# Kernel tuning notes

Hardware: AMD Instinct MI355X
Metric: run time of the kernel (lower is better)

Reference implementation:

```python
import jax, jax.numpy as jnp
import numpy as np
from jax import lax

L = 12        # transformer layers
H = 768       # d_model
NH = 12       # heads
HD = H // NH  # head dim
F = 2048      # ffn dim (torch TransformerEncoderLayer default)
V = 128       # vocab_size (level logits)
NLV = 128     # n_levels (rows of routed weight W)
B, S = 8, 512
EPS = 1e-5


def _layer_norm(x, g, b):
    mu = jnp.mean(x, axis=-1, keepdims=True)
    var = jnp.mean(jnp.square(x - mu), axis=-1, keepdims=True)
    return g * (x - mu) / jnp.sqrt(var + EPS) + b


def _encoder(x, layer_params):
    # torch nn.TransformerEncoderLayer, post-LN, ReLU, eval mode (no dropout)
    def block(h, p):
        Wqkv, bqkv, Wo, bo, g1, bb1, W1, b1f, W2, b2f, g2, bb2 = p
        qkv = h @ Wqkv.T + bqkv                      # [B,S,3H]
        q, k, v = jnp.split(qkv, 3, axis=-1)
        sh = (h.shape[0], h.shape[1], NH, HD)
        q, k, v = q.reshape(sh), k.reshape(sh), v.reshape(sh)
        scores = jnp.einsum('bqhd,bkhd->bhqk', q, k) / jnp.sqrt(jnp.asarray(HD, h.dtype))
        attn = jax.nn.softmax(scores, axis=-1)
        o = jnp.einsum('bhqk,bkhd->bqhd', attn, v).reshape(h.shape)
        o = o @ Wo.T + bo
        h = _layer_norm(h + o, g1, bb1)
        f = jnp.maximum(h @ W1.T + b1f, 0.0) @ W2.T + b2f
        h = _layer_norm(h + f, g2, bb2)
        return h, None
    x, _ = lax.scan(block, x, layer_params)
    return x


def setup_inputs() -> dict:
    key = jax.random.key(0)
    ks = jax.random.split(key, 20)
    s = 0.02
    rn = lambda k, shp: jax.random.normal(k, shp, jnp.float32) * s
    inp = {
        'level_ids': jax.random.randint(ks[0], (B, S), 0, V, jnp.int32),
        'sublevel_ids': jax.random.randint(ks[1], (B, S), 0, V, jnp.int32),
        'bin_emb': rn(ks[2], (V, H)),
        'sub_emb': rn(ks[3], (V, H)),
        'Wqkv': rn(ks[4], (L, 3 * H, H)),
        'bqkv': jnp.zeros((L, 3 * H), jnp.float32),
        'Wo': rn(ks[5], (L, H, H)),
        'bo': jnp.zeros((L, H), jnp.float32),
        'ln1_g': jnp.ones((L, H), jnp.float32),
        'ln1_b': jnp.zeros((L, H), jnp.float32),
        'W1': rn(ks[6], (L, F, H)),
        'b1': jnp.zeros((L, F), jnp.float32),
        'W2': rn(ks[7], (L, H, F)),
        'b2': jnp.zeros((L, H), jnp.float32),
        'ln2_g': jnp.ones((L, H), jnp.float32),
        'ln2_b': jnp.zeros((L, H), jnp.float32),
        'W_lm': rn(ks[8], (V, H)),
        'b_lm': jnp.zeros((V,), jnp.float32),
        'W': rn(ks[9], (NLV, H, V)),       # routed per-level weights
        'bias': jnp.zeros((NLV, V), jnp.float32),
    }
    return inp


def reference(level_ids, sublevel_ids, bin_emb, sub_emb, Wqkv, bqkv, Wo, bo,
              ln1_g, ln1_b, W1, b1, W2, b2, ln2_g, ln2_b, W_lm, b_lm, W, bias):
    # embedding: sum of two id tables (tabular bin/subbin embedding)
    x = bin_emb[level_ids] + sub_emb[sublevel_ids]            # [B,S,H]
    layer_params = (Wqkv, bqkv, Wo, bo, ln1_g, ln1_b, W1, b1, W2, b2, ln2_g, ln2_b)
    x = _encoder(x, layer_params)                              # [B,S,H]
    out = x @ W_lm.T + b_lm                                    # [B,S,V]
    ix = jnp.argmax(out, axis=-1)                              # [B,S] routing index
    # per-token weight gather + batched vec-mat: the irregular hot path
    Wg = W[ix]                                                 # [B,S,H,V]
    sublevel_out = jnp.einsum('bsh,bshv->bsv', x, Wg) + bias[ix]
    return (out, sublevel_out)
```

## Files before the change

kernel.cpp:

```cpp
#include <hip/hip_runtime.h>
#include <cstdint>
#include <cstddef>

#define TOK 4096
#define HD_ 64
#define NH_ 12
#define H_ 768
#define F_ 2048
#define V_ 128
#define L_ 12
#define SEQ 512
#define BQKV (3*H_)
#define BATCH 8

typedef _Float16 f16;
typedef _Float16 f16x8 __attribute__((ext_vector_type(8)));
typedef _Float16 f16x4 __attribute__((ext_vector_type(4)));
typedef float    f32x4 __attribute__((ext_vector_type(4)));

#define GLDS16(g, l) __builtin_amdgcn_global_load_lds( \
    (const __attribute__((address_space(1))) uint32_t*)(g), \
    (__attribute__((address_space(3))) uint32_t*)(l), 16, 0, 0)

__device__ __forceinline__ float wave_sum(float v) {
#pragma unroll
  for (int m = 32; m >= 1; m >>= 1) v += __shfl_xor(v, m);
  return v;
}

__device__ __forceinline__ void split16(float v, f16& h, f16& lo) {
  h = (f16)v;
  lo = (f16)((v - (float)h) * 2048.0f);
}

__device__ __forceinline__ int swz(int r, int c) {
  int byte = (r << 7) + (c << 1);
  byte ^= (r & 7) << 4;
  return byte >> 1;
}

__global__ __launch_bounds__(256)
void k_convert(const float* __restrict__ src, f16* __restrict__ h, f16* __restrict__ l,
               int n4, float scale) {
  int i = blockIdx.x * 256 + threadIdx.x;
  int stride = gridDim.x * 256;
  for (; i < n4; i += stride) {
    float4 v = ((const float4*)src)[i];
    v.x *= scale; v.y *= scale; v.z *= scale; v.w *= scale;
    f16x4 vh, vl;
    f16 a, b;
    split16(v.x, a, b); vh[0] = a; vl[0] = b;
    split16(v.y, a, b); vh[1] = a; vl[1] = b;
    split16(v.z, a, b); vh[2] = a; vl[2] = b;
    split16(v.w, a, b); vh[3] = a; vl[3] = b;
    ((f16x4*)h)[i] = vh;
    ((f16x4*)l)[i] = vl;
  }
}

__global__ __launch_bounds__(256)
void k_embed2(const int* __restrict__ lid, const int* __restrict__ sid,
              const float* __restrict__ be, const float* __restrict__ se,
              float* __restrict__ x, f16* __restrict__ xh, f16* __restrict__ xl,
              int* __restrict__ counts) {
  int t = blockIdx.x;
  if (t == 0 && threadIdx.x < V_) counts[threadIdx.x] = 0;
  int li = lid[t], si = sid[t];
  const float* bp = be + (size_t)li * H_;
  const float* sp = se + (size_t)si * H_;
  size_t base = (size_t)t * H_;
#pragma unroll
  for (int j = 0; j < 3; ++j) {
    int hh = threadIdx.x + 256 * j;
    float v = bp[hh] + sp[hh];
    x[base + hh] = v;
    f16 a, b; split16(v, a, b);
    xh[base + hh] = a; xl[base + hh] = b;
  }
}

template<int BM, int BN, int MODE>
__global__ __launch_bounds__(256)
void k_gemm4(const f16* __restrict__ Ah, const f16* __restrict__ Al,
             const f16* __restrict__ Bh, const f16* __restrict__ Bl,
             const float* __restrict__ bias, float* __restrict__ C,
             f16* __restrict__ Ch, f16* __restrict__ Cl,
             int N, int K) {
  constexpr int MI = BM / 32, NJ = BN / 32;
  constexpr int IA = BM / 64, IB = BN / 64;
  constexpr int ABYT = BM * 64, BBYT = BN * 64;
  constexpr int BUFB = 2 * ABYT + 2 * BBYT;
  constexpr int NGL = 2 * (IA + IB);
  __shared__ __align__(16) char sm_[3 * BUFB];
  const int tid = threadIdx.x;
  const int lane = tid & 63, wid = tid >> 6;
  const int wr = wid >> 1, wc = wid & 1;
  const int bm = blockIdx.x * BM, bn = blockIdx.y * BN;
  const size_t rs = (size_t)K * 2;

  const int srow = tid >> 2, schk = tid & 3;
  const char* ga[2][IA];
  const char* gb[2][IB];
#pragma unroll
  for (int u = 0; u < IA; ++u) {
    int row = u * 64 + srow;
    int c = schk ^ ((row >> 1) & 3);
    ga[0][u] = (const char*)Ah + (size_t)(bm + row) * rs + c * 16;
    ga[1][u] = (const char*)Al + (size_t)(bm + row) * rs + c * 16;
  }
#pragma unroll
  for (int u = 0; u < IB; ++u) {
    int row = u * 64 + srow;
    int c = schk ^ ((row >> 1) & 3);
    gb[0][u] = (const char*)Bh + (size_t)(bn + row) * rs + c * 16;
    gb[1][u] = (const char*)Bl + (size_t)(bn + row) * rs + c * 16;
  }

  const int rr = lane & 15, cgrp = lane >> 4;
  int aoff[MI][2], boff[NJ][2];
#pragma unroll
  for (int i = 0; i < MI; ++i) {
    int row = wr * (BM / 2) + i * 16 + rr;
    int sw = (cgrp ^ ((row >> 1) & 3)) * 16;
    aoff[i][0] = row * 64 + sw;
    aoff[i][1] = ABYT + row * 64 + sw;
  }
#pragma unroll
  for (int j = 0; j < NJ; ++j) {
    int row = wc * (BN / 2) + j * 16 + rr;
    int sw = (cgrp ^ ((row >> 1) & 3)) * 16;
    boff[j][0] = 2 * ABYT + row * 64 + sw;
    boff[j][1] = 2 * ABYT + BBYT + row * 64 + sw;
  }

  f32x4 aH[MI][NJ], aM[MI][NJ];
#pragma unroll
  for (int i = 0; i < MI; ++i)
#pragma unroll
    for (int j = 0; j < NJ; ++j)
#pragma unroll
      for (int q = 0; q < 4; ++q) { aH[i][j][q] = 0.0f; aM[i][j][q] = 0.0f; }

  auto STG = [&](char* bufbase) __attribute__((always_inline)) {
    char* base = bufbase + wid * 1024;
#pragma unroll
    for (int u = 0; u < IA; ++u) {
      GLDS16(ga[0][u], base + u * 4096);
      GLDS16(ga[1][u], base + ABYT + u * 4096);
      ga[0][u] += 64; ga[1][u] += 64;
    }
#pragma unroll
    for (int u = 0; u < IB; ++u) {
      GLDS16(gb[0][u], base + 2 * ABYT + u * 4096);
      GLDS16(gb[1][u], base + 2 * ABYT + BBYT + u * 4096);
      gb[0][u] += 64; gb[1][u] += 64;
    }
  };

  auto CMP = [&](const char* base) __attribute__((always_inline)) {
    f16x8 fbh[NJ], fbl[NJ];
#pragma unroll
    for (int j = 0; j < NJ; ++j) {
      fbh[j] = *(const f16x8*)(base + boff[j][0]);
      fbl[j] = *(const f16x8*)(base + boff[j][1]);
    }
#pragma unroll
    for (int i = 0; i < MI; ++i) {
      f16x8 fah = *(const f16x8*)(base + aoff[i][0]);
      f16x8 fal = *(const f16x8*)(base + aoff[i][1]);
#pragma unroll
      for (int j = 0; j < NJ; ++j) {
        aH[i][j] = __builtin_amdgcn_mfma_f32_16x16x32_f16(fah, fbh[j], aH[i][j], 0, 0, 0);
        aM[i][j] = __builtin_amdgcn_mfma_f32_16x16x32_f16(fah, fbl[j], aM[i][j], 0, 0, 0);
        aM[i][j] = __builtin_amdgcn_mfma_f32_16x16x32_f16(fal, fbh[j], aM[i][j], 0, 0, 0);
      }
    }
  };

  char* b0 = sm_;
  char* b1 = sm_ + BUFB;
  char* b2 = sm_ + 2 * BUFB;
  STG(b0);
  const int nst = K / 32;
  for (int s = 0; s < nst; ++s) {
    if (s + 1 < nst) {
      STG(b1);
      asm volatile("s_waitcnt vmcnt(%0)" :: "i"(NGL) : "memory");
    } else {
      asm volatile("s_waitcnt vmcnt(0)" ::: "memory");
    }
    __builtin_amdgcn_s_barrier();
    __builtin_amdgcn_sched_barrier(0);
    CMP(b0);
    char* tmp = b0; b0 = b1; b1 = b2; b2 = tmp;
  }

  const int r4 = (lane >> 4) * 4, cc = lane & 15;
#pragma unroll
  for (int i = 0; i < MI; ++i) {
#pragma unroll
    for (int j = 0; j < NJ; ++j) {
      int col = bn + wc * (BN / 2) + j * 16 + cc;
      float bz = bias[col];
#pragma unroll
      for (int q = 0; q < 4; ++q) {
        int row = bm + wr * (BM / 2) + i * 16 + r4 + q;
        float v = (aH[i][j][q] + aM[i][j][q] * (1.0f / 2048.0f)) * (1.0f / 64.0f) + bz;
        if (MODE == 0) {
          C[(size_t)row * N + col] = v;
        } else {
          if (MODE == 1) v = fmaxf(v, 0.0f);
          f16 a, b; split16(v, a, b);
          Ch[(size_t)row * N + col] = a;
          Cl[(size_t)row * N + col] = b;
        }
      }
    }
  }
}

__global__ __launch_bounds__(256)
void k_flash_mfma(const f16* __restrict__ ph, const f16* __restrict__ pl,
                  f16* __restrict__ oh, f16* __restrict__ ol) {
  __shared__ __align__(16) f16 VtH[4096];
  __shared__ __align__(16) f16 VtL[4096];
  __shared__ __align__(16) f16 PH[4096];
  __shared__ __align__(16) f16 PL[4096];
  __shared__ float PS[2][64];
  const int tid = threadIdx.x;
  const int lane = tid & 63, wid = tid >> 6;
  const int wr = wid >> 1, wc = wid & 1;
  const int qt = blockIdx.x, bh = blockIdx.y;
  const int b = bh / NH_, hd = bh % NH_;
  const int rr = lane & 15, kg = (lane >> 4) * 8;
  const size_t tok0 = (size_t)b * SEQ;

  f16x8 qfh[2][2], qfl[2][2];
#pragma unroll
  for (int ifr = 0; ifr < 2; ++ifr)
#pragma unroll
    for (int ks = 0; ks < 2; ++ks) {
      size_t g = (tok0 + qt * 64 + wr * 32 + ifr * 16 + rr) * (size_t)BQKV + hd * HD_ + ks * 32 + kg;
      qfh[ifr][ks] = *(const f16x8*)&ph[g];
      qfl[ifr][ks] = *(const f16x8*)&pl[g];
    }

  f32x4 oha[2][2], oma[2][2];
  f32x4 ps[2];
#pragma unroll
  for (int i = 0; i < 2; ++i) {
#pragma unroll
    for (int q = 0; q < 4; ++q) ps[i][q] = 0.0f;
#pragma unroll
    for (int j = 0; j < 2; ++j)
#pragma unroll
      for (int q = 0; q < 4; ++q) { oha[i][j][q] = 0.0f; oma[i][j][q] = 0.0f; }
  }

  const int vj = tid >> 2;
  const int vs = tid & 3;

  for (int kt = 0; kt < SEQ / 64; ++kt) {
    __syncthreads();
#pragma unroll
    for (int s = 0; s < 2; ++s) {
      int d0 = (vs + s * 4) * 8;
      size_t g = (tok0 + kt * 64 + vj) * (size_t)BQKV + 2 * H_ + hd * HD_ + d0;
      f16x8 vh8 = *(const f16x8*)&ph[g];
      f16x8 vl8 = *(const f16x8*)&pl[g];
#pragma unroll
      for (int u = 0; u < 8; ++u) {
        VtH[swz(d0 + u, vj)] = vh8[u];
        VtL[swz(d0 + u, vj)] = vl8[u];
      }
    }
    __syncthreads();
    f16x8 kfh[2][2], kfl[2][2];
#pragma unroll
    for (int jf = 0; jf < 2; ++jf)
#pragma unroll
      for (int ks = 0; ks < 2; ++ks) {
        size_t g = (tok0 + kt * 64 + wc * 32 + jf * 16 + rr) * (size_t)BQKV + H_ + hd * HD_ + ks * 32 + kg;
        kfh[jf][ks] = *(const f16x8*)&ph[g];
        kfl[jf][ks] = *(const f16x8*)&pl[g];
      }
    f32x4 sh[2][2], sm2[2][2];
#pragma unroll
    for (int i = 0; i < 2; ++i)
#pragma unroll
      for (int j = 0; j < 2; ++j)
#pragma unroll
        for (int q = 0; q < 4; ++q) { sh[i][j][q] = 0.0f; sm2[i][j][q] = 0.0f; }
#pragma unroll
    for (int ifr = 0; ifr < 2; ++ifr)
#pragma unroll
      for (int jf = 0; jf < 2; ++jf)
#pragma unroll
        for (int ks = 0; ks < 2; ++ks) {
          sh[ifr][jf] = __builtin_amdgcn_mfma_f32_16x16x32_f16(qfh[ifr][ks], kfh[jf][ks], sh[ifr][jf], 0, 0, 0);
          sm2[ifr][jf] = __builtin_amdgcn_mfma_f32_16x16x32_f16(qfh[ifr][ks], kfl[jf][ks], sm2[ifr][jf], 0, 0, 0);
          sm2[ifr][jf] = __builtin_amdgcn_mfma_f32_16x16x32_f16(qfl[ifr][ks], kfh[jf][ks], sm2[ifr][jf], 0, 0, 0);
        }
#pragma unroll
    for (int ifr = 0; ifr < 2; ++ifr)
#pragma unroll
      for (int jf = 0; jf < 2; ++jf) {
        int pj = wc * 32 + jf * 16 + rr;
#pragma unroll
        for (int q = 0; q < 4; ++q) {
          int pi = wr * 32 + ifr * 16 + (lane >> 4) * 4 + q;
          float sval = (sh[ifr][jf][q] + sm2[ifr][jf][q] * (1.0f / 2048.0f)) * 0.125f;
          float p = expf(sval);
          ps[ifr][q] += p;
          f16 a, b2; split16(p, a, b2);
          PH[swz(pi, pj)] = a;
          PL[swz(pi, pj)] = b2;
        }
      }
    __syncthreads();
#pragma unroll
    for (int ks = 0; ks < 2; ++ks) {
      f16x8 pfh[2], pfl[2], vfh[2], vfl[2];
#pragma unroll
      for (int ifr = 0; ifr < 2; ++ifr) {
        pfh[ifr] = *(const f16x8*)&PH[swz(wr * 32 + ifr * 16 + rr, ks * 32 + kg)];
        pfl[ifr] = *(const f16x8*)&PL[swz(wr * 32 + ifr * 16 + rr, ks * 32 + kg)];
      }
#pragma unroll
      for (int jf = 0; jf < 2; ++jf) {
        vfh[jf] = *(const f16x8*)&VtH[swz(wc * 32 + jf * 16 + rr, ks * 32 + kg)];
        vfl[jf] = *(const f16x8*)&VtL[swz(wc * 32 + jf * 16 + rr, ks * 32 + kg)];
      }
#pragma unroll
      for (int ifr = 0; ifr < 2; ++ifr)
#pragma unroll
        for (int jf = 0; jf < 2; ++jf) {
          oha[ifr][jf] = __builtin_amdgcn_mfma_f32_16x16x32_f16(pfh[ifr], vfh[jf], oha[ifr][jf], 0, 0, 0);
          oma[ifr][jf] = __builtin_amdgcn_mfma_f32_16x16x32_f16(pfh[ifr], vfl[jf], oma[ifr][jf], 0, 0, 0);
          oma[ifr][jf] = __builtin_amdgcn_mfma_f32_16x16x32_f16(pfl[ifr], vfh[jf], oma[ifr][jf], 0, 0, 0);
        }
    }
  }

#pragma unroll
  for (int ifr = 0; ifr < 2; ++ifr)
#pragma unroll
    for (int m = 1; m < 16; m <<= 1)
#pragma unroll
      for (int q = 0; q < 4; ++q) ps[ifr][q] += __shfl_xor(ps[ifr][q], m);
  if (rr == 0) {
#pragma unroll
    for (int ifr = 0; ifr < 2; ++ifr)
#pragma unroll
      for (int q = 0; q < 4; ++q)
        PS[wc][wr * 32 + ifr * 16 + (lane >> 4) * 4 + q] = ps[ifr][q];
  }
  __syncthreads();

#pragma unroll
  for (int ifr = 0; ifr < 2; ++ifr)
#pragma unroll
    for (int jf = 0; jf < 2; ++jf)
#pragma unroll
      for (int q = 0; q < 4; ++q) {
        int i = wr * 32 + ifr * 16 + (lane >> 4) * 4 + q;
        float inv = 1.0f / (PS[0][i] + PS[1][i]);
        float o = (oha[ifr][jf][q] + oma[ifr][jf][q] * (1.0f / 2048.0f)) * inv;
        size_t g = (tok0 + qt * 64 + i) * (size_t)H_ + hd * HD_ + wc * 32 + jf * 16 + rr;
        f16 a, b2; split16(o, a, b2);
        oh[g] = a; ol[g] = b2;
      }
}

__global__ __launch_bounds__(256)
void k_ln_res2(const float* __restrict__ xin, const float* __restrict__ y,
               const float* __restrict__ g, const float* __restrict__ bb,
               float* __restrict__ xout, f16* __restrict__ xh, f16* __restrict__ xl) {
  __shared__ float red[8];
  int t = blockIdx.x;
  const float* xr = xin + (size_t)t * H_;
  const float* yr = y + (size_t)t * H_;
  float v[3];
#pragma unroll
  for (int j = 0; j < 3; ++j) {
    int hh = threadIdx.x + 256 * j;
    v[j] = xr[hh] + yr[hh];
  }
  float s = v[0] + v[1] + v[2];
  s = wave_sum(s);
  int w = threadIdx.x >> 6;
  if ((threadIdx.x & 63) == 0) red[w] = s;
  __syncthreads();
  float mu = (red[0] + red[1] + red[2] + red[3]) * (1.0f / 768.0f);
  float q = 0.f;
#pragma unroll
  for (int j = 0; j < 3; ++j) { float d = v[j] - mu; q = fmaf(d, d, q); }
  q = wave_sum(q);
  if ((threadIdx.x & 63) == 0) red[4 + w] = q;
  __syncthreads();
  float var = (red[4] + red[5] + red[6] + red[7]) * (1.0f / 768.0f);
  float rinv = 1.0f / sqrtf(var + 1e-5f);
#pragma unroll
  for (int j = 0; j < 3; ++j) {
    int hh = threadIdx.x + 256 * j;
    float val = fmaf(g[hh], (v[j] - mu) * rinv, bb[hh]);
    size_t idx = (size_t)t * H_ + hh;
    xout[idx] = val;
    f16 a, b; split16(val, a, b);
    xh[idx] = a; xl[idx] = b;
  }
}

__global__ __launch_bounds__(64)
void k_argmax(const float* __restrict__ logits, int* __restrict__ ix,
              int* __restrict__ counts) {
  int t = blockIdx.x, l = threadIdx.x;
  float v0 = logits[(size_t)t * V_ + l];
  float v1 = logits[(size_t)t * V_ + 64 + l];
  float best = v0; int bi = l;
  if (v1 > best) { best = v1; bi = 64 + l; }
#pragma unroll
  for (int m = 1; m < 64; m <<= 1) {
    float ov = __shfl_xor(best, m);
    int oi = __shfl_xor(bi, m);
    if (ov > best || (ov == best && oi < bi)) { best = ov; bi = oi; }
  }
  if (l == 0) { ix[t] = bi; atomicAdd(&counts[bi], 1); }
}

__global__ __launch_bounds__(128)
void k_prep(const int* __restrict__ counts, int* __restrict__ offsets,
            int* __restrict__ cursors, int4* __restrict__ chunks,
            int* __restrict__ nchunks) {
  __shared__ int s[128];
  int r = threadIdx.x;
  int c = counts[r];
  s[r] = c; __syncthreads();
  for (int d = 1; d < 128; d <<= 1) {
    int v = (r >= d) ? s[r - d] : 0; __syncthreads();
    s[r] += v; __syncthreads();
  }
  int off = s[r] - c;
  offsets[r] = off;
  cursors[r] = 0;
  int nch = (c + 15) >> 4;
  __syncthreads();
  s[r] = nch; __syncthreads();
  for (int d = 1; d < 128; d <<= 1) {
    int v = (r >= d) ? s[r - d] : 0; __syncthreads();
    s[r] += v; __syncthreads();
  }
  int cb = s[r] - nch;
  for (int u = 0; u < nch; ++u) {
    int rem = c - u * 16;
    chunks[cb + u] = make_int4(r, off + u * 16, rem < 16 ? rem : 16, 0);
  }
  if (r == 127) *nchunks = s[127];
}

__global__ __launch_bounds__(256)
void k_scatter(const int* __restrict__ ix, const int* __restrict__ offsets,
               int* __restrict__ cursors, int* __restrict__ bucket) {
  int t = blockIdx.x * 256 + threadIdx.x;
  int r = ix[t];
  int p = atomicAdd(&cursors[r], 1);
  bucket[offsets[r] + p] = t;
}

__global__ __launch_bounds__(256)
void k_sublevel2(const float* __restrict__ x, const float* __restrict__ W,
                 const float* __restrict__ bias, const int* __restrict__ bucket,
                 const int4* __restrict__ chunks, const int* __restrict__ nchunks,
                 float* __restrict__ out) {
  int c = blockIdx.x;
  if (c >= *nchunks) return;
  int4 ch = chunks[c];
  int r = ch.x, ts = ch.y, nt = ch.z;
  __shared__ int toks[16];
  __shared__ float accs[16][V_];
  int tid = threadIdx.x;
  if (tid < 16) toks[tid] = bucket[ts + (tid < nt ? tid : 0)];
  __syncthreads();
  const int lane = tid & 63;
  const int wv = tid >> 6;
  const int vh = wv & 1, kh = wv >> 1;
  const int v = vh * 64 + lane;
  const float* Wr = W + (size_t)r * (H_ * V_);
  int tk[16];
#pragma unroll
  for (int t = 0; t < 16; ++t) tk[t] = toks[t];
  float acc[16];
#pragma unroll
  for (int t = 0; t < 16; ++t) acc[t] = 0.f;

  for (int k0 = kh * 384; k0 < kh * 384 + 384; k0 += 64) {
    float xv[16];
#pragma unroll
    for (int t = 0; t < 16; ++t)
      xv[t] = x[(size_t)tk[t] * H_ + k0 + lane];
#pragma unroll 4
    for (int kk = 0; kk < 64; ++kk) {
      float w = Wr[(size_t)(k0 + kk) * V_ + v];
#pragma unroll
      for (int t = 0; t < 16; ++t) {
        float xs = __uint_as_float(
            __builtin_amdgcn_readlane(__float_as_uint(xv[t]), kk));
        acc[t] = fmaf(xs, w, acc[t]);
      }
    }
  }
  if (kh == 1) {
#pragma unroll
    for (int t = 0; t < 16; ++t) accs[t][v] = acc[t];
  }
  __syncthreads();
  if (kh == 0) {
    float bz = bias[(size_t)r * V_ + v];
#pragma unroll
    for (int t = 0; t < 16; ++t) {
      if (t < nt) out[(size_t)tk[t] * V_ + v] = acc[t] + accs[t][v] + bz;
    }
  }
}

extern "C" void kernel_launch(void* const* d_in, const int* in_sizes, int n_in,
                              void* d_out, int out_size, void* d_ws, size_t ws_size,
                              hipStream_t stream) {
  const int*   lid  = (const int*)d_in[0];
  const int*   sid  = (const int*)d_in[1];
  const float* be   = (const float*)d_in[2];
  const float* se   = (const float*)d_in[3];
  const float* Wqkv = (const float*)d_in[4];
  const float* bqkv = (const float*)d_in[5];
  const float* Wo   = (const float*)d_in[6];
  const float* bo   = (const float*)d_in[7];
  const float* g1   = (const float*)d_in[8];
  const float* b1n  = (const float*)d_in[9];
  const float* W1   = (const float*)d_in[10];
  const float* b1f  = (const float*)d_in[11];
  const float* W2   = (const float*)d_in[12];
  const float* b2f  = (const float*)d_in[13];
  const float* g2   = (const float*)d_in[14];
  const float* b2n  = (const float*)d_in[15];
  const float* Wlm  = (const float*)d_in[16];
  const float* blm  = (const float*)d_in[17];
  const float* Wrt  = (const float*)d_in[18];
  const float* brt  = (const float*)d_in[19];

  char* ws = (char*)d_ws;
  float* x    = (float*)(ws + 0);
  f16*   xh   = (f16*)  (ws + 12582912);
  f16*   xl   = (f16*)  (ws + 18874368);
  f16*   qh   = (f16*)  (ws + 25165824);
  f16*   ql   = (f16*)  (ws + 44040192);
  f16*   midh = qh;
  f16*   midl = ql;
  f16*   ath  = (f16*)  (ws + 62914560);
  f16*   atl  = (f16*)  (ws + 69206016);
  float* bufY = (float*)(ws + 75497472);
  f16*   wsh  = (f16*)  (ws + 88080384);
  f16*   wsl  = (f16*)  (ws + 91619328);
  f16*   wlmh = (f16*)  (ws + 95158272);
  f16*   wlml = (f16*)  (ws + 95354880);
  int*   ix   = (int*)  (ws + 95551488);
  int*   counts  = (int*)(ws + 95567872);
  int*   cursors = (int*)(ws + 95568384);
  int*   offsets = (int*)(ws + 95568896);
  int4*  chunks  = (int4*)(ws + 95569920);
  int*   nchunks = (int*)(ws + 95576064);
  int*   bucket  = (int*)(ws + 95576320);
  const size_t need = 95592704;
  if (ws_size < need) return;

  bool big = ws_size >= 95600640ull + 265000000ull;
  f16 *bWqh = nullptr, *bWql = nullptr, *bWoh = nullptr, *bWol = nullptr,
      *bW1h = nullptr, *bW1l = nullptr, *bW2h = nullptr, *bW2l = nullptr;
  if (big) {
    char* p = ws + 95600640;
    bWqh = (f16*)p; p += 42467328;
    bWql = (f16*)p; p += 42467328;
    bWoh = (f16*)p; p += 14155776;
    bWol = (f16*)p; p += 14155776;
    bW1h = (f16*)p; p += 37748736;
    bW1l = (f16*)p; p += 37748736;
    bW2h = (f16*)p; p += 37748736;
    bW2l = (f16*)p; p += 37748736;
    k_convert<<<2048, 256, 0, stream>>>(Wqkv, bWqh, bWql, L_ * BQKV * H_ / 4, 64.f);
    k_convert<<<2048, 256, 0, stream>>>(Wo,   bWoh, bWol, L_ * H_ * H_ / 4, 64.f);
    k_convert<<<2048, 256, 0, stream>>>(W1,   bW1h, bW1l, L_ * F_ * H_ / 4, 64.f);
    k_convert<<<2048, 256, 0, stream>>>(W2,   bW2h, bW2l, L_ * H_ * F_ / 4, 64.f);
  }
  k_convert<<<96, 256, 0, stream>>>(Wlm, wlmh, wlml, V_ * H_ / 4, 64.f);

  float* out0 = (float*)d_out;
  float* out1 = out0 + (size_t)TOK * V_;

  k_embed2<<<TOK, 256, 0, stream>>>(lid, sid, be, se, x, xh, xl, counts);

  for (int l = 0; l < L_; ++l) {
    const float* bqkv_l = bqkv + (size_t)l * BQKV;
    const float* bo_l   = bo   + (size_t)l * H_;
    const float* g1_l   = g1   + (size_t)l * H_;
    const float* b1n_l  = b1n  + (size_t)l * H_;
    const float* b1f_l  = b1f  + (size_t)l * F_;
    const float* b2f_l  = b2f  + (size_t)l * H_;
    const float* g2_l   = g2   + (size_t)l * H_;
    const float* b2n_l  = b2n  + (size_t)l * H_;

    const f16 *wh, *wl2;
    if (big) { wh = bWqh + (size_t)l * BQKV * H_; wl2 = bWql + (size_t)l * BQKV * H_; }
    else {
      k_convert<<<1728, 256, 0, stream>>>(Wqkv + (size_t)l * BQKV * H_, wsh, wsl, BQKV * H_ / 4, 64.f);
      wh = wsh; wl2 = wsl;
    }
    k_gemm4<64, 128, 2><<<dim3(TOK / 64, BQKV / 128), 256, 0, stream>>>(
        xh, xl, wh, wl2, bqkv_l, nullptr, qh, ql, BQKV, H_);
    k_flash_mfma<<<dim3(SEQ / 64, BATCH * NH_), 256, 0, stream>>>(qh, ql, ath, atl);
    if (big) { wh = bWoh + (size_t)l * H_ * H_; wl2 = bWol + (size_t)l * H_ * H_; }
    else {
      k_convert<<<576, 256, 0, stream>>>(Wo + (size_t)l * H_ * H_, wsh, wsl, H_ * H_ / 4, 64.f);
      wh = wsh; wl2 = wsl;
    }
    k_gemm4<64, 64, 0><<<dim3(TOK / 64, H_ / 64), 256, 0, stream>>>(
        ath, atl, wh, wl2, bo_l, bufY, nullptr, nullptr, H_, H_);
    k_ln_res2<<<TOK, 256, 0, stream>>>(x, bufY, g1_l, b1n_l, x, xh, xl);
    if (big) { wh = bW1h + (size_t)l * F_ * H_; wl2 = bW1l + (size_t)l * F_ * H_; }
    else {
      k_convert<<<1536, 256, 0, stream>>>(W1 + (size_t)l * F_ * H_, wsh, wsl, F_ * H_ / 4, 64.f);
      wh = wsh; wl2 = wsl;
    }
    k_gemm4<64, 128, 1><<<dim3(TOK / 64, F_ / 128), 256, 0, stream>>>(
        xh, xl, wh, wl2, b1f_l, nullptr, midh, midl, F_, H_);
    if (big) { wh = bW2h + (size_t)l * H_ * F_; wl2 = bW2l + (size_t)l * H_ * F_; }
    else {
      k_convert<<<1536, 256, 0, stream>>>(W2 + (size_t)l * H_ * F_, wsh, wsl, H_ * F_ / 4, 64.f);
      wh = wsh; wl2 = wsl;
    }
    k_gemm4<64, 64, 0><<<dim3(TOK / 64, H_ / 64), 256, 0, stream>>>(
        midh, midl, wh, wl2, b2f_l, bufY, nullptr, nullptr, H_, F_);
    k_ln_res2<<<TOK, 256, 0, stream>>>(x, bufY, g2_l, b2n_l, x, xh, xl);
  }

  k_gemm4<64, 64, 0><<<dim3(TOK / 64, V_ / 64), 256, 0, stream>>>(
      xh, xl, wlmh, wlml, blm, out0, nullptr, nullptr, V_, H_);
  k_argmax<<<TOK, 64, 0, stream>>>(out0, ix, counts);
  k_prep<<<1, 128, 0, stream>>>(counts, offsets, cursors, chunks, nchunks);
  k_scatter<<<TOK / 256, 256, 0, stream>>>(ix, offsets, cursors, bucket);
  k_sublevel2<<<384, 256, 0, stream>>>(x, Wrt, brt, bucket, chunks, nchunks, out1);
}
```

Baseline: 3.696 ms.

## Split-K the narrow GEMMs with fused reduction and move sublevel matvec to MFMA

The Wo, W2 and LM-head GEMMs now split K across blockIdx.z and write partial sums to workspace. The following layernorm or argmax kernel reduces the partials and adds the bias. This raises the block count for the 768- and 128-wide outputs, which otherwise launch few blocks, at the cost of extra partial-buffer traffic. Separately, the routed per-level weights are transposed and split into f16 hi/lo pairs, and the sublevel vec-mat is redone with MFMA instead of scalar FMAs with readlane. That adds a conversion pass over the 128x768x128 weight each call.

```diff
diff --git a/kernel.cpp b/kernel.cpp
--- a/kernel.cpp
+++ b/kernel.cpp
@@ -79,7 +79,7 @@
   }
 }
 
-template<int BM, int BN, int MODE>
+template<int BM, int BN, int MODE, int SPLIT>
 __global__ __launch_bounds__(256)
 void k_gemm4(const f16* __restrict__ Ah, const f16* __restrict__ Al,
              const f16* __restrict__ Bh, const f16* __restrict__ Bl,
@@ -97,6 +97,7 @@
   const int wr = wid >> 1, wc = wid & 1;
   const int bm = blockIdx.x * BM, bn = blockIdx.y * BN;
   const size_t rs = (size_t)K * 2;
+  const size_t koff = (size_t)blockIdx.z * (size_t)(K / SPLIT) * 2;
 
   const int srow = tid >> 2, schk = tid & 3;
   const char* ga[2][IA];
@@ -105,15 +106,15 @@
   for (int u = 0; u < IA; ++u) {
     int row = u * 64 + srow;
     int c = schk ^ ((row >> 1) & 3);
-    ga[0][u] = (const char*)Ah + (size_t)(bm + row) * rs + c * 16;
-    ga[1][u] = (const char*)Al + (size_t)(bm + row) * rs + c * 16;
+    ga[0][u] = (const char*)Ah + (size_t)(bm + row) * rs + c * 16 + koff;
+    ga[1][u] = (const char*)Al + (size_t)(bm + row) * rs + c * 16 + koff;
   }
 #pragma unroll
   for (int u = 0; u < IB; ++u) {
     int row = u * 64 + srow;
     int c = schk ^ ((row >> 1) & 3);
-    gb[0][u] = (const char*)Bh + (size_t)(bn + row) * rs + c * 16;
-    gb[1][u] = (const char*)Bl + (size_t)(bn + row) * rs + c * 16;
+    gb[0][u] = (const char*)Bh + (size_t)(bn + row) * rs + c * 16 + koff;
+    gb[1][u] = (const char*)Bl + (size_t)(bn + row) * rs + c * 16 + koff;
   }
 
   const int rr = lane & 15, cgrp = lane >> 4;
@@ -181,7 +182,7 @@
   char* b1 = sm_ + BUFB;
   char* b2 = sm_ + 2 * BUFB;
   STG(b0);
-  const int nst = K / 32;
+  const int nst = (K / SPLIT) / 32;
   for (int s = 0; s < nst; ++s) {
     if (s + 1 < nst) {
       STG(b1);
@@ -196,18 +197,19 @@
   }
 
   const int r4 = (lane >> 4) * 4, cc = lane & 15;
+  float* Cp = (MODE == 3) ? (C + (size_t)blockIdx.z * ((size_t)TOK * N)) : C;
 #pragma unroll
   for (int i = 0; i < MI; ++i) {
 #pragma unroll
     for (int j = 0; j < NJ; ++j) {
       int col = bn + wc * (BN / 2) + j * 16 + cc;
-      float bz = bias[col];
+      float bz = (MODE == 3) ? 0.0f : bias[col];
 #pragma unroll
       for (int q = 0; q < 4; ++q) {
         int row = bm + wr * (BM / 2) + i * 16 + r4 + q;
         float v = (aH[i][j][q] + aM[i][j][q] * (1.0f / 2048.0f)) * (1.0f / 64.0f) + bz;
-        if (MODE == 0) {
-          C[(size_t)row * N + col] = v;
+        if (MODE == 0 || MODE == 3) {
+          Cp[(size_t)row * N + col] = v;
         } else {
           if (MODE == 1) v = fmaxf(v, 0.0f);
           f16 a, b; split16(v, a, b);
@@ -373,18 +375,20 @@
 }
 
 __global__ __launch_bounds__(256)
-void k_ln_res2(const float* __restrict__ xin, const float* __restrict__ y,
+void k_ln_res3(const float* __restrict__ xin, const float* __restrict__ part,
+               const float* __restrict__ bcol,
                const float* __restrict__ g, const float* __restrict__ bb,
                float* __restrict__ xout, f16* __restrict__ xh, f16* __restrict__ xl) {
   __shared__ float red[8];
   int t = blockIdx.x;
   const float* xr = xin + (size_t)t * H_;
-  const float* yr = y + (size_t)t * H_;
+  const float* p0 = part + (size_t)t * H_;
+  const float* p1 = part + (size_t)TOK * H_ + (size_t)t * H_;
   float v[3];
 #pragma unroll
   for (int j = 0; j < 3; ++j) {
     int hh = threadIdx.x + 256 * j;
-    v[j] = xr[hh] + yr[hh];
+    v[j] = xr[hh] + ((p0[hh] + p1[hh]) + bcol[hh]);
   }
   float s = v[0] + v[1] + v[2];
   s = wave_sum(s);
@@ -412,11 +416,17 @@
 }
 
 __global__ __launch_bounds__(64)
-void k_argmax(const float* __restrict__ logits, int* __restrict__ ix,
-              int* __restrict__ counts) {
+void k_argmax2(const float* __restrict__ part, const float* __restrict__ blm,
+               float* __restrict__ out0, int* __restrict__ ix,
+               int* __restrict__ counts) {
   int t = blockIdx.x, l = threadIdx.x;
-  float v0 = logits[(size_t)t * V_ + l];
-  float v1 = logits[(size_t)t * V_ + 64 + l];
+  const size_t S = (size_t)TOK * V_;
+  size_t c0 = (size_t)t * V_ + l;
+  size_t c1 = c0 + 64;
+  float v0 = ((part[c0] + part[S + c0]) + part[2 * S + c0]) + part[3 * S + c0] + blm[l];
+  float v1 = ((part[c1] + part[S + c1]) + part[2 * S + c1]) + part[3 * S + c1] + blm[l + 64];
+  out0[c0] = v0;
+  out0[c1] = v1;
   float best = v0; int bi = l;
   if (v1 > best) { best = v1; bi = 64 + l; }
 #pragma unroll
@@ -468,7 +478,34 @@
 }
 
 __global__ __launch_bounds__(256)
-void k_sublevel2(const float* __restrict__ x, const float* __restrict__ W,
+void k_convT(const float* __restrict__ W, f16* __restrict__ wth, f16* __restrict__ wtl) {
+  __shared__ float tile[64][65];
+  const int r = blockIdx.x, vb = blockIdx.y * 64;
+  const int tid = threadIdx.x;
+  const int la = tid & 63, wv = tid >> 6;
+  for (int ht = 0; ht < H_ / 64; ++ht) {
+    int h0 = ht * 64;
+#pragma unroll
+    for (int i = 0; i < 16; ++i) {
+      int row = wv + i * 4;
+      tile[row][la] = W[(size_t)r * (H_ * V_) + (size_t)(h0 + row) * V_ + vb + la];
+    }
+    __syncthreads();
+#pragma unroll
+    for (int i = 0; i < 16; ++i) {
+      int vl = wv + i * 4;
+      float w = tile[la][vl];
+      f16 a, b; split16(w, a, b);
+      size_t o = ((size_t)r * V_ + vb + vl) * H_ + h0 + la;
+      wth[o] = a; wtl[o] = b;
+    }
+    __syncthreads();
+  }
+}
+
+__global__ __launch_bounds__(256)
+void k_sublevel3(const f16* __restrict__ xh, const f16* __restrict__ xl,
+                 const f16* __restrict__ wth, const f16* __restrict__ wtl,
                  const float* __restrict__ bias, const int* __restrict__ bucket,
                  const int4* __restrict__ chunks, const int* __restrict__ nchunks,
                  float* __restrict__ out) {
@@ -477,48 +514,49 @@
   int4 ch = chunks[c];
   int r = ch.x, ts = ch.y, nt = ch.z;
   __shared__ int toks[16];
-  __shared__ float accs[16][V_];
   int tid = threadIdx.x;
   if (tid < 16) toks[tid] = bucket[ts + (tid < nt ? tid : 0)];
   __syncthreads();
-  const int lane = tid & 63;
-  const int wv = tid >> 6;
-  const int vh = wv & 1, kh = wv >> 1;
-  const int v = vh * 64 + lane;
-  const float* Wr = W + (size_t)r * (H_ * V_);
-  int tk[16];
-#pragma unroll
-  for (int t = 0; t < 16; ++t) tk[t] = toks[t];
-  float acc[16];
-#pragma unroll
-  for (int t = 0; t < 16; ++t) acc[t] = 0.f;
-
-  for (int k0 = kh * 384; k0 < kh * 384 + 384; k0 += 64) {
-    float xv[16];
-#pragma unroll
-    for (int t = 0; t < 16; ++t)
-      xv[t] = x[(size_t)tk[t] * H_ + k0 + lane];
-#pragma unroll 4
-    for (int kk = 0; kk < 64; ++kk) {
-      float w = Wr[(size_t)(k0 + kk) * V_ + v];
-#pragma unroll
-      for (int t = 0; t < 16; ++t) {
-        float xs = __uint_as_float(
-            __builtin_amdgcn_readlane(__float_as_uint(xv[t]), kk));
-        acc[t] = fmaf(xs, w, acc[t]);
-      }
-    }
-  }
-  if (kh == 1) {
-#pragma unroll
-    for (int t = 0; t < 16; ++t) accs[t][v] = acc[t];
-  }
-  __syncthreads();
-  if (kh == 0) {
-    float bz = bias[(size_t)r * V_ + v];
-#pragma unroll
-    for (int t = 0; t < 16; ++t) {
-      if (t < nt) out[(size_t)tk[t] * V_ + v] = acc[t] + accs[t][v] + bz;
+  const int lane = tid & 63, wid = tid >> 6;
+  const int rr = lane & 15, kg = (lane >> 4) * 8;
+  const int myTok = toks[rr];
+  const size_t abase = (size_t)myTok * H_ + kg;
+
+  f32x4 aH[2], aM[2];
+#pragma unroll
+  for (int j = 0; j < 2; ++j)
+#pragma unroll
+    for (int q = 0; q < 4; ++q) { aH[j][q] = 0.0f; aM[j][q] = 0.0f; }
+
+  size_t wb[2];
+#pragma unroll
+  for (int j = 0; j < 2; ++j)
+    wb[j] = ((size_t)r * V_ + wid * 32 + j * 16 + rr) * H_ + kg;
+
+  for (int k0 = 0; k0 < H_; k0 += 32) {
+    f16x8 ah = *(const f16x8*)&xh[abase + k0];
+    f16x8 al = *(const f16x8*)&xl[abase + k0];
+#pragma unroll
+    for (int j = 0; j < 2; ++j) {
+      f16x8 bh = *(const f16x8*)&wth[wb[j] + k0];
+      f16x8 bl = *(const f16x8*)&wtl[wb[j] + k0];
+      aH[j] = __builtin_amdgcn_mfma_f32_16x16x32_f16(ah, bh, aH[j], 0, 0, 0);
+      aM[j] = __builtin_amdgcn_mfma_f32_16x16x32_f16(ah, bl, aM[j], 0, 0, 0);
+      aM[j] = __builtin_amdgcn_mfma_f32_16x16x32_f16(al, bh, aM[j], 0, 0, 0);
+    }
+  }
+
+  const int r4 = (lane >> 4) * 4, cc = lane & 15;
+#pragma unroll
+  for (int j = 0; j < 2; ++j) {
+#pragma unroll
+    for (int q = 0; q < 4; ++q) {
+      int row = r4 + q;
+      if (row < nt) {
+        int col = wid * 32 + j * 16 + cc;
+        out[(size_t)toks[row] * V_ + col] =
+            aH[j][q] + aM[j][q] * (1.0f / 2048.0f) + bias[(size_t)r * V_ + col];
+      }
     }
   }
 }
@@ -558,6 +596,11 @@
   f16*   ath  = (f16*)  (ws + 62914560);
   f16*   atl  = (f16*)  (ws + 69206016);
   float* bufY = (float*)(ws + 75497472);
+  float* pO   = (float*)(ws + 25165824);
+  float* pF   = (float*)(ws + 62914560);
+  float* pLM  = bufY;
+  f16*   wth  = (f16*)  (ws + 25165824);
+  f16*   wtl  = (f16*)  (ws + 50331648);
   f16*   wsh  = (f16*)  (ws + 88080384);
   f16*   wsl  = (f16*)  (ws + 91619328);
   f16*   wlmh = (f16*)  (ws + 95158272);
@@ -613,7 +656,7 @@
       k_convert<<<1728, 256, 0, stream>>>(Wqkv + (size_t)l * BQKV * H_, wsh, wsl, BQKV * H_ / 4, 64.f);
       wh = wsh; wl2 = wsl;
     }
-    k_gemm4<64, 128, 2><<<dim3(TOK / 64, BQKV / 128), 256, 0, stream>>>(
+    k_gemm4<64, 128, 2, 1><<<dim3(TOK / 64, BQKV / 128, 1), 256, 0, stream>>>(
         xh, xl, wh, wl2, bqkv_l, nullptr, qh, ql, BQKV, H_);
     k_flash_mfma<<<dim3(SEQ / 64, BATCH * NH_), 256, 0, stream>>>(qh, ql, ath, atl);
     if (big) { wh = bWoh + (size_t)l * H_ * H_; wl2 = bWol + (size_t)l * H_ * H_; }
@@ -621,30 +664,31 @@
       k_convert<<<576, 256, 0, stream>>>(Wo + (size_t)l * H_ * H_, wsh, wsl, H_ * H_ / 4, 64.f);
       wh = wsh; wl2 = wsl;
     }
-    k_gemm4<64, 64, 0><<<dim3(TOK / 64, H_ / 64), 256, 0, stream>>>(
-        ath, atl, wh, wl2, bo_l, bufY, nullptr, nullptr, H_, H_);
-    k_ln_res2<<<TOK, 256, 0, stream>>>(x, bufY, g1_l, b1n_l, x, xh, xl);
+    k_gemm4<64, 64, 3, 2><<<dim3(TOK / 64, H_ / 64, 2), 256, 0, stream>>>(
+        ath, atl, wh, wl2, nullptr, pO, nullptr, nullptr, H_, H_);
+    k_ln_res3<<<TOK, 256, 0, stream>>>(x, pO, bo_l, g1_l, b1n_l, x, xh, xl);
     if (big) { wh = bW1h + (size_t)l * F_ * H_; wl2 = bW1l + (size_t)l * F_ * H_; }
     else {
       k_convert<<<1536, 256, 0, stream>>>(W1 + (size_t)l * F_ * H_, wsh, wsl, F_ * H_ / 4, 64.f);
       wh = wsh; wl2 = wsl;
     }
-    k_gemm4<64, 128, 1><<<dim3(TOK / 64, F_ / 128), 256, 0, stream>>>(
+    k_gemm4<64, 128, 1, 1><<<dim3(TOK / 64, F_ / 128, 1), 256, 0, stream>>>(
         xh, xl, wh, wl2, b1f_l, nullptr, midh, midl, F_, H_);
     if (big) { wh = bW2h + (size_t)l * H_ * F_; wl2 = bW2l + (size_t)l * H_ * F_; }
     else {
       k_convert<<<1536, 256, 0, stream>>>(W2 + (size_t)l * H_ * F_, wsh, wsl, H_ * F_ / 4, 64.f);
       wh = wsh; wl2 = wsl;
     }
-    k_gemm4<64, 64, 0><<<dim3(TOK / 64, H_ / 64), 256, 0, stream>>>(
-        midh, midl, wh, wl2, b2f_l, bufY, nullptr, nullptr, H_, F_);
-    k_ln_res2<<<TOK, 256, 0, stream>>>(x, bufY, g2_l, b2n_l, x, xh, xl);
-  }
-
-  k_gemm4<64, 64, 0><<<dim3(TOK / 64, V_ / 64), 256, 0, stream>>>(
-      xh, xl, wlmh, wlml, blm, out0, nullptr, nullptr, V_, H_);
-  k_argmax<<<TOK, 64, 0, stream>>>(out0, ix, counts);
+    k_gemm4<64, 64, 3, 2><<<dim3(TOK / 64, H_ / 64, 2), 256, 0, stream>>>(
+        midh, midl, wh, wl2, nullptr, pF, nullptr, nullptr, H_, F_);
+    k_ln_res3<<<TOK, 256, 0, stream>>>(x, pF, b2f_l, g2_l, b2n_l, x, xh, xl);
+  }
+
+  k_gemm4<64, 64, 3, 4><<<dim3(TOK / 64, V_ / 64, 4), 256, 0, stream>>>(
+      xh, xl, wlmh, wlml, nullptr, pLM, nullptr, nullptr, V_, H_);
+  k_convT<<<dim3(V_, 2), 256, 0, stream>>>(Wrt, wth, wtl);
+  k_argmax2<<<TOK, 64, 0, stream>>>(pLM, blm, out0, ix, counts);
   k_prep<<<1, 128, 0, stream>>>(counts, offsets, cursors, chunks, nchunks);
   k_scatter<<<TOK / 256, 256, 0, stream>>>(ix, offsets, cursors, bucket);
-  k_sublevel2<<<384, 256, 0, stream>>>(x, Wrt, brt, bucket, chunks, nchunks, out1);
-}
+  k_sublevel3<<<384, 256, 0, stream>>>(xh, xl, wth, wtl, brt, bucket, chunks, nchunks, out1);
+}
```

Result: no change. 3.697 ms (+0.0%).
